# Kernel tuning notes

Hardware: AMD Instinct MI355X
Metric: run time of the kernel (lower is better)

The kernel has to match this reference:

```python
import jax, jax.numpy as jnp
import numpy as np

N, E, G = 50000, 800000, 16
NODE, HID, OUT, HEADS = 128, 64, 128, 3
NEG_SLOPE = 0.2

def setup_inputs() -> dict:
    key = jax.random.key(0)
    ks = jax.random.split(key, 12)
    h = jax.random.normal(ks[0], (N, NODE), jnp.float32)
    z = jax.random.normal(ks[1], (G, OUT), jnp.float32)
    src = jax.random.randint(ks[2], (E,), 0, N, jnp.int32)
    dst = jax.random.randint(ks[3], (E,), 0, N, jnp.int32)
    graph_id = jnp.sort(jax.random.randint(ks[4], (N,), 0, G, jnp.int32))
    s = 0.1
    fc_w = jax.random.normal(ks[5], (HEADS * HID, NODE), jnp.float32) * s
    attn_l = jax.random.normal(ks[6], (HEADS, HID), jnp.float32) * s
    attn_r = jax.random.normal(ks[7], (HEADS, HID), jnp.float32) * s
    bias = jnp.zeros((HEADS * HID,), jnp.float32)
    lin1_w = jax.random.normal(ks[8], (HID, OUT), jnp.float32) * s
    lin1_b = jnp.zeros((HID,), jnp.float32)
    lin2_w = jax.random.normal(ks[9], (1, 2 * HID), jnp.float32) * s
    lin2_b = jnp.zeros((1,), jnp.float32)
    return dict(h=h, z=z, src=src, dst=dst, graph_id=graph_id, fc_w=fc_w,
                attn_l=attn_l, attn_r=attn_r, bias=bias,
                lin1_w=lin1_w, lin1_b=lin1_b, lin2_w=lin2_w, lin2_b=lin2_b)

def reference(h, z, src, dst, graph_id, fc_w, attn_l, attn_r, bias,
              lin1_w, lin1_b, lin2_w, lin2_b):
    n = h.shape[0]
    # GATConv: projection -> [N, H, D]
    feat = (h @ fc_w.T).reshape(n, HEADS, HID)
    el = jnp.sum(feat * attn_l, axis=-1)  # [N, H]
    er = jnp.sum(feat * attn_r, axis=-1)  # [N, H]
    e = jax.nn.leaky_relu(el[src] + er[dst], NEG_SLOPE)  # [E, H]
    # edge softmax per destination node
    m = jax.ops.segment_max(e, dst, num_segments=n)
    e = jnp.exp(e - m[dst])
    s = jax.ops.segment_sum(e, dst, num_segments=n)
    alpha = e / s[dst]
    # scatter-weighted aggregation
    msg = alpha[:, :, None] * feat[src]  # [E, H, D]
    rst = jax.ops.segment_sum(msg, dst, num_segments=n)  # [N, H, D]
    rst = rst + bias.reshape(HEADS, HID)
    h_d = jnp.mean(rst, axis=1)  # [N, D] (mean over heads)
    # dgl.mean_nodes: per-graph mean pooling
    counts = jax.ops.segment_sum(jnp.ones((n,), h_d.dtype), graph_id, num_segments=G)
    pooled = jax.ops.segment_sum(h_d, graph_id, num_segments=G) / jnp.maximum(counts, 1.0)[:, None]
    z1 = z @ lin1_w.T + lin1_b  # [G, HID]
    cat = jnp.concatenate([pooled, z1], axis=1)  # [G, 2*HID]
    score = jax.nn.sigmoid(cat @ lin2_w.T + lin2_b)  # [G, 1]
    return score
```

## Files before the change

kernel.cpp:

```cpp
#include <hip/hip_runtime.h>
#include <math.h>

#define N_NODES 50000
#define N_EDGES 800000
#define N_GRAPHS 16
#define NODE_F 128
#define HID 64
#define OUT_F 128
#define HEADS 3
#define NEG 0.2f
#define FEAT (HEADS*HID)

typedef float f32x4 __attribute__((ext_vector_type(4)));
typedef float f32x2 __attribute__((ext_vector_type(2)));
typedef short bf16x8 __attribute__((ext_vector_type(8)));

#if defined(__has_builtin)
#if __has_builtin(__builtin_amdgcn_cvt_pk_f32_fp8) && __has_builtin(__builtin_amdgcn_cvt_pk_fp8_f32)
#define USE_FP8 1
#endif
#endif
#ifndef USE_FP8
#define USE_FP8 0
#endif

#if USE_FP8
#define FB 1
#else
#define FB 2
#endif
#define GRP (8 * FB)
#define ROW (32 * GRP)

#define NBKT ((N_NODES + 63) / 64)
#define H1B 400
#define EPB (N_EDGES / H1B)

__device__ __forceinline__ ushort f2bf(float x) {
  union { float f; unsigned u; } v; v.f = x;
  unsigned r = v.u + 0x7fff + ((v.u >> 16) & 1);
  return (ushort)(r >> 16);
}
__device__ __forceinline__ float bf2f(ushort x) {
  union { unsigned u; float f; } v; v.u = ((unsigned)x) << 16;
  return v.f;
}

__device__ __forceinline__ void feat_store(unsigned char* base, int n, int hh, int dd, float v) {
  size_t off = (size_t)n * ROW + (dd >> 1) * GRP + ((hh * 2 + (dd & 1)) * FB);
#if USE_FP8
  base[off] = (unsigned char)(__builtin_amdgcn_cvt_pk_fp8_f32(v, 0.f, 0, false) & 0xff);
#else
  *(ushort*)(base + off) = f2bf(v);
#endif
}

#define ZERO_INTS (N_GRAPHS * HID + N_GRAPHS)
#define ZERO_U4 (ZERO_INTS / 4)
#define ZB ((ZERO_U4 + 255) / 256)
__global__ void kprep(const float* __restrict__ fc_w, ushort* __restrict__ fcb,
                      uint4* __restrict__ zbase) {
  if (blockIdx.x >= 24) {
    int i = (blockIdx.x - 24) * 256 + threadIdx.x;
    if (i < ZERO_U4) zbase[i] = make_uint4(0, 0, 0, 0);
    return;
  }
  int i = blockIdx.x * 256 + threadIdx.x;
  int col = i >> 5;
  int kb = (i & 31) * 4;
  float4 v = *(const float4*)(fc_w + (size_t)col * NODE_F + kb);
  int t = col >> 4, m = col & 15;
  int kk = kb >> 5, kq = (kb >> 3) & 3, j = kb & 7;
  size_t idx0 = ((((size_t)t * 4 + kk) * 4 + kq) * 16 + m) * 8 + j;
  ushort4 o; o.x = f2bf(v.x); o.y = f2bf(v.y); o.z = f2bf(v.z); o.w = f2bf(v.w);
  *(ushort4*)(fcb + idx0) = o;
}

#define GB0 ((N_NODES + 63) / 64)
__global__ __launch_bounds__(256) void k01_fused(
    const float* __restrict__ h, const ushort* __restrict__ fcb,
    const float* __restrict__ attn_l, const float* __restrict__ attn_r,
    const int* __restrict__ dst,
    unsigned char* __restrict__ feat, float* __restrict__ el, float* __restrict__ er,
    int* __restrict__ cnt_g)
{
  __shared__ ushort A[64][136];
  const int tid = threadIdx.x;

  if (blockIdx.x < H1B) {
    int* cnt = (int*)&A[0][0];
    const int blk = blockIdx.x;
    for (int i = tid; i < NBKT; i += 256) cnt[i] = 0;
    __syncthreads();
    const int e0 = blk * EPB;
    for (int i = tid; i < EPB; i += 256)
      atomicAdd(&cnt[dst[e0 + i] >> 6], 1);
    __syncthreads();
    for (int i = tid; i < NBKT; i += 256) cnt_g[(size_t)blk * NBKT + i] = cnt[i];
    return;
  }

  const int n0 = (blockIdx.x - H1B) * 64;
  for (int i = tid; i < 64 * 32; i += 256) {
    int r = i >> 5, c4 = i & 31;
    if (n0 + r < N_NODES) {
      float4 v = *(const float4*)(h + (size_t)(n0 + r) * NODE_F + c4 * 4);
      unsigned lo = f2bf(v.x) | ((unsigned)f2bf(v.y) << 16);
      unsigned hi = f2bf(v.z) | ((unsigned)f2bf(v.w) << 16);
      *(uint2*)&A[r][c4 * 4] = make_uint2(lo, hi);
    }
  }
  __syncthreads();

  const int lane = tid & 63, wv = tid >> 6;
  const int m = lane & 15, kq = lane >> 4;

  f32x4 acc[12];
#pragma unroll
  for (int t = 0; t < 12; t++) acc[t] = (f32x4){0.f, 0.f, 0.f, 0.f};

#pragma unroll
  for (int kk = 0; kk < 4; kk++) {
    bf16x8 af = *(const bf16x8*)&A[wv * 16 + m][kk * 32 + kq * 8];
#pragma unroll
    for (int t = 0; t < 12; t++) {
      const bf16x8 bf = *(const bf16x8*)(fcb + ((((size_t)t * 4 + kk) * 4 + kq) * 16 + m) * 8);
      acc[t] = __builtin_amdgcn_mfma_f32_16x16x32_bf16(af, bf, acc[t], 0, 0, 0);
    }
  }

  const int rbase = n0 + wv * 16 + kq * 4;
#pragma unroll
  for (int t = 0; t < 12; t++) {
    const int hh = t >> 2;
    const int dd = (t & 3) * 16 + m;
#pragma unroll
    for (int reg = 0; reg < 4; reg++) {
      int n = rbase + reg;
      if (n < N_NODES) feat_store(feat, n, hh, dd, acc[t][reg]);
    }
  }

#pragma unroll
  for (int hh = 0; hh < HEADS; hh++) {
    float elv[4] = {0.f, 0.f, 0.f, 0.f};
    float erv[4] = {0.f, 0.f, 0.f, 0.f};
#pragma unroll
    for (int tt = 0; tt < 4; tt++) {
      int t = hh * 4 + tt;
      float al = attn_l[hh * HID + tt * 16 + m];
      float ar = attn_r[hh * HID + tt * 16 + m];
#pragma unroll
      for (int reg = 0; reg < 4; reg++) {
        elv[reg] = fmaf(acc[t][reg], al, elv[reg]);
        erv[reg] = fmaf(acc[t][reg], ar, erv[reg]);
      }
    }
#pragma unroll
    for (int reg = 0; reg < 4; reg++) {
#pragma unroll
      for (int off = 1; off < 16; off <<= 1) {
        elv[reg] += __shfl_xor(elv[reg], off, 64);
        erv[reg] += __shfl_xor(erv[reg], off, 64);
      }
      int n = rbase + reg;
      if (m == 0 && n < N_NODES) {
        el[(size_t)n * 4 + hh] = elv[reg];
        er[(size_t)n * 4 + hh] = erv[reg];
      }
    }
  }
}

#define H2A_K 7
__global__ __launch_bounds__(64) void kh2a_scan(
    const int* __restrict__ cnt_g, int* __restrict__ base_bm, int* __restrict__ btot)
{
  const int b = blockIdx.x;
  const int lane = threadIdx.x;
  int v[H2A_K];
  int lt = 0;
#pragma unroll
  for (int j = 0; j < H2A_K; j++) {
    int g = lane * H2A_K + j;
    v[j] = (g < H1B) ? cnt_g[(size_t)g * NBKT + b] : 0;
    lt += v[j];
  }
  int s = lt;
#pragma unroll
  for (int off = 1; off < 64; off <<= 1) {
    int t = __shfl_up(s, off, 64);
    if (lane >= off) s += t;
  }
  int excl = s - lt;
#pragma unroll
  for (int j = 0; j < H2A_K; j++) {
    int g = lane * H2A_K + j;
    if (g < H1B) base_bm[(size_t)b * H1B + g] = excl;
    excl += v[j];
  }
  if (lane == 63) btot[b] = s;
}

__global__ __launch_bounds__(256) void kh3_scatter(
    const int* __restrict__ src, const int* __restrict__ dst,
    const int* __restrict__ btot, const int* __restrict__ base_bm,
    int2* __restrict__ pairs)
{
  __shared__ int cur[NBKT];
  __shared__ int wsum[4];
  const int tid = threadIdx.x, blk = blockIdx.x;
  const int lane = tid & 63, wv = tid >> 6;
  int v[4]; int lt = 0;
#pragma unroll
  for (int j = 0; j < 4; j++) {
    int g = tid * 4 + j;
    v[j] = (g < NBKT) ? btot[g] : 0;
    lt += v[j];
  }
  int s = lt;
#pragma unroll
  for (int off = 1; off < 64; off <<= 1) {
    int t = __shfl_up(s, off, 64);
    if (lane >= off) s += t;
  }
  if (lane == 63) wsum[wv] = s;
  __syncthreads();
  int woff = 0;
#pragma unroll
  for (int w = 0; w < 4; w++) woff += (w < wv) ? wsum[w] : 0;
  int excl = s - lt + woff;
#pragma unroll
  for (int j = 0; j < 4; j++) {
    int g = tid * 4 + j;
    if (g < NBKT) cur[g] = excl + base_bm[(size_t)g * H1B + blk];
    excl += v[j];
  }
  __syncthreads();
  const int e0 = blk * EPB;
  for (int i = tid; i < EPB; i += 256) {
    int e = e0 + i;
    int d = dst[e], sv = src[e];
    int slot = atomicAdd(&cur[d >> 6], 1);
    pairs[slot] = make_int2(sv, d);
  }
}

__global__ __launch_bounds__(256) void kh4_nodesort(
    const int2* __restrict__ pairs, const int* __restrict__ btot,
    int* __restrict__ src_s, int* __restrict__ offs)
{
  __shared__ int nodecnt[64];
  __shared__ int cur[64];
  __shared__ int red_[4];
  __shared__ int lo_s, hi_s;
  const int b = blockIdx.x, tid = threadIdx.x;
  const int lane = tid & 63, wv = tid >> 6;
  int partial = 0;
  for (int i = tid; i < b; i += 256) partial += btot[i];
#pragma unroll
  for (int off = 32; off; off >>= 1) partial += __shfl_xor(partial, off, 64);
  if (lane == 0) red_[wv] = partial;
  if (tid < 64) nodecnt[tid] = 0;
  __syncthreads();
  if (tid == 0) {
    int l = red_[0] + red_[1] + red_[2] + red_[3];
    lo_s = l; hi_s = l + btot[b];
  }
  __syncthreads();
  const int lo = lo_s, hi = hi_s;
  for (int i = lo + tid; i < hi; i += 256)
    atomicAdd(&nodecnt[pairs[i].y & 63], 1);
  __syncthreads();
  if (tid < 64) {
    int v = nodecnt[tid];
    int s = v;
#pragma unroll
    for (int off = 1; off < 64; off <<= 1) {
      int t = __shfl_up(s, off, 64);
      if (tid >= off) s += t;
    }
    int excl = s - v;
    cur[tid] = lo + excl;
    int n = b * 64 + tid;
    if (n < N_NODES) offs[n] = lo + excl;
    if (b == NBKT - 1 && tid == 0) offs[N_NODES] = N_EDGES;
  }
  __syncthreads();
  for (int i = lo + tid; i < hi; i += 256) {
    int2 pr = pairs[i];
    int slot = atomicAdd(&cur[pr.y & 63], 1);
    src_s[slot] = pr.x;
  }
}

__global__ __launch_bounds__(256) void k4_agg(
    const int* __restrict__ offs, const int* __restrict__ src_s,
    const float* __restrict__ el4, const float* __restrict__ er4,
    const unsigned char* __restrict__ feat, const float* __restrict__ bias,
    float* __restrict__ h_d)
{
  __shared__ float4 rec[4][64];
  const int wv = threadIdx.x >> 6, lane = threadIdx.x & 63;
  const int n = blockIdx.x * 4 + wv;
  const int lo = offs[n], hi = offs[n + 1];
  const int half = lane >> 5;
  const int d = lane & 31;
  const char* fb = (const char*)feat;
  const float4 ern = ((const float4*)er4)[n];

  float a0x = 0.f, a0y = 0.f, a1x = 0.f, a1y = 0.f, a2x = 0.f, a2y = 0.f;
  float s0 = 0.f, s1 = 0.f, s2 = 0.f;

  for (int base = lo; base < hi; base += 64) {
    const int cnt = min(64, hi - base);
    if (lane < cnt) {
      int sidx = src_s[base + lane];
      float4 elv = ((const float4*)el4)[sidx];
      float e0 = elv.x + ern.x; e0 = e0 > 0.f ? e0 : NEG * e0;
      float e1 = elv.y + ern.y; e1 = e1 > 0.f ? e1 : NEG * e1;
      float e2 = elv.z + ern.z; e2 = e2 > 0.f ? e2 : NEG * e2;
      float4 c;
      c.x = __expf(e0); c.y = __expf(e1); c.z = __expf(e2);
      c.w = __int_as_float(sidx * ROW);
      rec[wv][lane] = c;
      s0 += c.x; s1 += c.y; s2 += c.z;
    }
#define K4_BODY(J) do { \
      float4 c = rec[wv][J]; \
      const char* rp = fb + __float_as_int(c.w) + GRP * d; \
      f32x2 f0, f1, f2; \
      if (USE_FP8) { \
        uint2 q = *(const uint2*)rp; \
        f0 = __builtin_amdgcn_cvt_pk_f32_fp8(q.x & 0xffff, false); \
        f1 = __builtin_amdgcn_cvt_pk_f32_fp8(q.x >> 16, false); \
        f2 = __builtin_amdgcn_cvt_pk_f32_fp8(q.y & 0xffff, false); \
      } else { \
        uint4 q = *(const uint4*)rp; \
        f0.x = bf2f((ushort)(q.x & 0xffff)); f0.y = bf2f((ushort)(q.x >> 16)); \
        f1.x = bf2f((ushort)(q.y & 0xffff)); f1.y = bf2f((ushort)(q.y >> 16)); \
        f2.x = bf2f((ushort)(q.z & 0xffff)); f2.y = bf2f((ushort)(q.z >> 16)); \
      } \
      a0x = fmaf(c.x, f0.x, a0x); a0y = fmaf(c.x, f0.y, a0y); \
      a1x = fmaf(c.y, f1.x, a1x); a1y = fmaf(c.y, f1.y, a1y); \
      a2x = fmaf(c.z, f2.x, a2x); a2y = fmaf(c.z, f2.y, a2y); \
    } while (0)
    int j = half;
    for (; j + 2 < cnt; j += 4) { K4_BODY(j); K4_BODY(j + 2); }
    if (j < cnt) K4_BODY(j);
#undef K4_BODY
  }
  a0x += __shfl_xor(a0x, 32, 64); a0y += __shfl_xor(a0y, 32, 64);
  a1x += __shfl_xor(a1x, 32, 64); a1y += __shfl_xor(a1y, 32, 64);
  a2x += __shfl_xor(a2x, 32, 64); a2y += __shfl_xor(a2y, 32, 64);
#pragma unroll
  for (int off = 32; off; off >>= 1) {
    s0 += __shfl_xor(s0, off, 64);
    s1 += __shfl_xor(s1, off, 64);
    s2 += __shfl_xor(s2, off, 64);
  }
  const float i0 = s0 > 0.f ? 1.f / s0 : 0.f;
  const float i1 = s1 > 0.f ? 1.f / s1 : 0.f;
  const float i2 = s2 > 0.f ? 1.f / s2 : 0.f;
  if (half == 0) {
    float2 b0 = *(const float2*)(bias + 2 * d);
    float2 b1 = *(const float2*)(bias + HID + 2 * d);
    float2 b2 = *(const float2*)(bias + 2 * HID + 2 * d);
    float2 o;
    o.x = (fmaf(a0x, i0, b0.x) + fmaf(a1x, i1, b1.x) + fmaf(a2x, i2, b2.x)) * (1.f / 3.f);
    o.y = (fmaf(a0y, i0, b0.y) + fmaf(a1y, i1, b1.y) + fmaf(a2y, i2, b2.y)) * (1.f / 3.f);
    *(float2*)(h_d + (size_t)n * HID + 2 * d) = o;
  }
}

#define K5_NPB 128
#define K5_NB ((N_NODES + K5_NPB - 1) / K5_NPB)
#define NSEG (K5_NB * 2)
__global__ __launch_bounds__(256) void k5a_partial(
    const int* __restrict__ graph_id, const float* __restrict__ h_d,
    float* __restrict__ pooled_res, int* __restrict__ gcnt_res,
    float* __restrict__ part, int* __restrict__ pg, int* __restrict__ pc)
{
  const int wv = threadIdx.x >> 6, lane = threadIdx.x & 63;
  const int b = blockIdx.x;
  const int n0 = b * K5_NPB;
  const int n1 = min(n0 + K5_NPB, N_NODES);
  const int g_lo = graph_id[n0], g_hi = graph_id[n1 - 1];

  if (g_hi > g_lo + 1) {
    float acc = 0.f; int cur_g = -1; int cnt = 0;
    for (int i = n0 + wv; i < n1; i += 4) {
      int g = graph_id[i];
      if (g != cur_g) {
        if (cur_g >= 0) {
          atomicAdd(&pooled_res[cur_g * HID + lane], acc);
          if (lane == 0) atomicAdd(&gcnt_res[cur_g], cnt);
        }
        acc = 0.f; cnt = 0; cur_g = g;
      }
      acc += h_d[(size_t)i * HID + lane];
      cnt++;
    }
    if (cur_g >= 0) {
      atomicAdd(&pooled_res[cur_g * HID + lane], acc);
      if (lane == 0) atomicAdd(&gcnt_res[cur_g], cnt);
    }
    if (threadIdx.x < 2) pg[b * 2 + threadIdx.x] = -1;
    return;
  }

  float acc_lo = 0.f, acc_hi = 0.f;
  int c_lo = 0, c_hi = 0;
  for (int i = n0 + wv; i < n1; i += 4) {
    int g = graph_id[i];
    float v = h_d[(size_t)i * HID + lane];
    bool hi = (g != g_lo);
    acc_hi += hi ? v : 0.f;
    acc_lo += hi ? 0.f : v;
    c_hi += hi ? 1 : 0;
    c_lo += hi ? 0 : 1;
  }
  __shared__ float ls[2][4][64];
  __shared__ int lc[2][4];
  ls[0][wv][lane] = acc_lo;
  ls[1][wv][lane] = acc_hi;
  if (lane == 0) { lc[0][wv] = c_lo; lc[1][wv] = c_hi; }
  __syncthreads();
  if (wv < 2) {
    float s = ls[wv][0][lane] + ls[wv][1][lane] + ls[wv][2][lane] + ls[wv][3][lane];
    part[((size_t)b * 2 + wv) * HID + lane] = s;
    if (lane == 0) {
      int cnt = lc[wv][0] + lc[wv][1] + lc[wv][2] + lc[wv][3];
      int gg = (wv == 0) ? g_lo : g_hi;
      if (wv == 1 && (g_hi == g_lo || cnt == 0)) gg = -1;
      pg[b * 2 + wv] = gg;
      pc[b * 2 + wv] = cnt;
    }
  }
}

__global__ __launch_bounds__(256) void k6_final(
    const float* __restrict__ part, const int* __restrict__ pg, const int* __restrict__ pc,
    const float* __restrict__ pooled_res, const int* __restrict__ gcnt_res,
    const float* __restrict__ z,
    const float* __restrict__ lin1_w, const float* __restrict__ lin1_b,
    const float* __restrict__ lin2_w, const float* __restrict__ lin2_b,
    float* __restrict__ out)
{
  const int g = blockIdx.x;
  const int tid = threadIdx.x, wv = tid >> 6, lane = tid & 63;
  __shared__ int spg[NSEG], spc[NSEG];
  __shared__ float red[4][HID];
  __shared__ int rc[4];
  __shared__ float cat[2 * HID];

  for (int i = tid; i < NSEG; i += 256) { spg[i] = pg[i]; spc[i] = pc[i]; }
  __syncthreads();

  float acc = 0.f; int cnt = 0;
  for (int s = wv; s < NSEG; s += 4) {
    if (spg[s] == g) {
      acc += part[(size_t)s * HID + lane];
      cnt += spc[s];
    }
  }
  red[wv][lane] = acc;
  if (lane == 0) rc[wv] = cnt;
  __syncthreads();

  if (wv == 0) {
    float s = red[0][lane] + red[1][lane] + red[2][lane] + red[3][lane]
            + pooled_res[g * HID + lane];
    int c = rc[0] + rc[1] + rc[2] + rc[3] + gcnt_res[g];
    cat[lane] = s / (float)(c > 0 ? c : 1);
  }
  if (wv == 1) {
    float s = lin1_b[lane];
    const float* zr = z + g * OUT_F;
    const float* wr = lin1_w + lane * OUT_F;
    for (int k = 0; k < OUT_F; k += 4) {
      float4 zv = *(const float4*)(zr + k);
      float4 wv4 = *(const float4*)(wr + k);
      s = fmaf(zv.x, wv4.x, fmaf(zv.y, wv4.y, fmaf(zv.z, wv4.z, fmaf(zv.w, wv4.w, s))));
    }
    cat[HID + lane] = s;
  }
  __syncthreads();
  if (wv == 0) {
    float s = cat[lane] * lin2_w[lane] + cat[HID + lane] * lin2_w[HID + lane];
#pragma unroll
    for (int off = 32; off; off >>= 1) s += __shfl_xor(s, off, 64);
    if (lane == 0) out[g] = 1.f / (1.f + __expf(-(s + lin2_b[0])));
  }
}

extern "C" void kernel_launch(void* const* d_in, const int* in_sizes, int n_in,
                              void* d_out, int out_size, void* d_ws, size_t ws_size,
                              hipStream_t stream) {
  (void)in_sizes; (void)n_in; (void)out_size; (void)ws_size;
  const float* h      = (const float*)d_in[0];
  const float* z      = (const float*)d_in[1];
  const int*   src    = (const int*)d_in[2];
  const int*   dst    = (const int*)d_in[3];
  const int*   gid    = (const int*)d_in[4];
  const float* fc_w   = (const float*)d_in[5];
  const float* attn_l = (const float*)d_in[6];
  const float* attn_r = (const float*)d_in[7];
  const float* bias   = (const float*)d_in[8];
  const float* lin1_w = (const float*)d_in[9];
  const float* lin1_b = (const float*)d_in[10];
  const float* lin2_w = (const float*)d_in[11];
  const float* lin2_b = (const float*)d_in[12];
  float* out = (float*)d_out;

  int2* pairs       = (int2*)d_ws;
  unsigned char* feat = (unsigned char*)(pairs + N_EDGES);
  float* h_d        = (float*)(feat + (size_t)N_NODES * ROW);
  float* el         = h_d + (size_t)N_NODES * HID;
  float* er         = el + (size_t)N_NODES * 4;
  float* part       = er + (size_t)N_NODES * 4;
  int* pg           = (int*)(part + (size_t)NSEG * HID);
  int* pc           = pg + NSEG;
  ushort* fcb       = (ushort*)(pc + NSEG);
  float* pooled_res = (float*)(fcb + 192 * NODE_F);
  int* gcnt_res     = (int*)(pooled_res + N_GRAPHS * HID);
  int* offs         = gcnt_res + N_GRAPHS;
  int* src_s        = offs + (N_NODES + 1);
  int* cnt_g        = src_s + N_EDGES;
  int* base_bm      = cnt_g + (size_t)H1B * NBKT;
  int* btot         = base_bm + (size_t)NBKT * H1B;

  kprep<<<24 + ZB, 256, 0, stream>>>(fc_w, fcb, (uint4*)pooled_res);
  k01_fused<<<H1B + GB0, 256, 0, stream>>>(h, fcb, attn_l, attn_r, dst,
                                           feat, el, er, cnt_g);
  kh2a_scan<<<NBKT, 64, 0, stream>>>(cnt_g, base_bm, btot);
  kh3_scatter<<<H1B, 256, 0, stream>>>(src, dst, btot, base_bm, pairs);
  kh4_nodesort<<<NBKT, 256, 0, stream>>>(pairs, btot, src_s, offs);
  k4_agg<<<N_NODES / 4, 256, 0, stream>>>(offs, src_s, el, er, feat, bias, h_d);
  k5a_partial<<<K5_NB, 256, 0, stream>>>(gid, h_d, pooled_res, gcnt_res, part, pg, pc);
  k6_final<<<N_GRAPHS, 256, 0, stream>>>(part, pg, pc, pooled_res, gcnt_res,
                                         z, lin1_w, lin1_b, lin2_w, lin2_b, out);
}
```

Measured before the change: 206.1 us.

## Fuse node sort, aggregation and pooling into one bucket-per-block kernel

```diff
diff --git a/kernel.cpp b/kernel.cpp
--- a/kernel.cpp
+++ b/kernel.cpp
@@ -35,6 +35,8 @@
 #define NBKT ((N_NODES + 63) / 64)
 #define H1B 400
 #define EPB (N_EDGES / H1B)
+#define NSEG (NBKT * 2)
+#define MAXE 2048
 
 __device__ __forceinline__ ushort f2bf(float x) {
   union { float f; unsigned u; } v; v.f = x;
@@ -246,31 +248,52 @@
   }
 }
 
-__global__ __launch_bounds__(256) void kh4_nodesort(
+#define K4W 8
+__global__ __launch_bounds__(512) void k4_big(
     const int2* __restrict__ pairs, const int* __restrict__ btot,
-    int* __restrict__ src_s, int* __restrict__ offs)
+    const int* __restrict__ gid,
+    const float* __restrict__ el4, const float* __restrict__ er4,
+    const unsigned char* __restrict__ feat, const float* __restrict__ bias,
+    float* __restrict__ pooled_res, int* __restrict__ gcnt_res,
+    float* __restrict__ part, int* __restrict__ pg, int* __restrict__ pc,
+    int* __restrict__ src_ovf)
 {
-  __shared__ int nodecnt[64];
-  __shared__ int cur[64];
-  __shared__ int red_[4];
-  __shared__ int lo_s, hi_s;
+  __shared__ int ssrc[MAXE];
+  __shared__ int nodecnt[64], noff[64], cur[64];
+  __shared__ int red_[K4W];
+  __shared__ int lo_s;
+  __shared__ float4 rec[K4W][64];
+  __shared__ float pool[K4W][2][HID];
+  __shared__ int pooln[K4W][2];
   const int b = blockIdx.x, tid = threadIdx.x;
   const int lane = tid & 63, wv = tid >> 6;
+
   int partial = 0;
-  for (int i = tid; i < b; i += 256) partial += btot[i];
+  for (int i = tid; i < b; i += 512) partial += btot[i];
 #pragma unroll
   for (int off = 32; off; off >>= 1) partial += __shfl_xor(partial, off, 64);
   if (lane == 0) red_[wv] = partial;
   if (tid < 64) nodecnt[tid] = 0;
+  if (tid < 64) { pool[tid >> 6][0][lane] = 0.f; }
   __syncthreads();
   if (tid == 0) {
-    int l = red_[0] + red_[1] + red_[2] + red_[3];
-    lo_s = l; hi_s = l + btot[b];
-  }
-  __syncthreads();
-  const int lo = lo_s, hi = hi_s;
-  for (int i = lo + tid; i < hi; i += 256)
-    atomicAdd(&nodecnt[pairs[i].y & 63], 1);
+    int l = 0;
+#pragma unroll
+    for (int w = 0; w < K4W; w++) l += red_[w];
+    lo_s = l;
+  }
+  if (tid < 512) {
+    int w = tid >> 6;
+    pool[w][0][lane] = 0.f;
+    pool[w][1][lane] = 0.f;
+    if (lane == 0) { pooln[w][0] = 0; pooln[w][1] = 0; }
+  }
+  __syncthreads();
+  const int lo = lo_s;
+  const int cnt = btot[b];
+
+  for (int i = tid; i < cnt; i += 512)
+    atomicAdd(&nodecnt[pairs[lo + i].y & 63], 1);
   __syncthreads();
   if (tid < 64) {
     int v = nodecnt[tid];
@@ -280,52 +303,54 @@
       int t = __shfl_up(s, off, 64);
       if (tid >= off) s += t;
     }
-    int excl = s - v;
-    cur[tid] = lo + excl;
-    int n = b * 64 + tid;
-    if (n < N_NODES) offs[n] = lo + excl;
-    if (b == NBKT - 1 && tid == 0) offs[N_NODES] = N_EDGES;
-  }
-  __syncthreads();
-  for (int i = lo + tid; i < hi; i += 256) {
-    int2 pr = pairs[i];
+    noff[tid] = s - v;
+    cur[tid] = s - v;
+  }
+  __syncthreads();
+  int* slist = (cnt <= MAXE) ? (int*)ssrc : (src_ovf + lo);
+  for (int i = tid; i < cnt; i += 512) {
+    int2 pr = pairs[lo + i];
     int slot = atomicAdd(&cur[pr.y & 63], 1);
-    src_s[slot] = pr.x;
-  }
-}
-
-__global__ __launch_bounds__(256) void k4_agg(
-    const int* __restrict__ offs, const int* __restrict__ src_s,
-    const float* __restrict__ el4, const float* __restrict__ er4,
-    const unsigned char* __restrict__ feat, const float* __restrict__ bias,
-    float* __restrict__ h_d)
-{
-  __shared__ float4 rec[4][64];
-  const int wv = threadIdx.x >> 6, lane = threadIdx.x & 63;
-  const int n = blockIdx.x * 4 + wv;
-  const int lo = offs[n], hi = offs[n + 1];
+    slist[slot] = pr.x;
+  }
+  __syncthreads();
+
+  const int g_lo = gid[b * 64];
+  const int nlast = min(b * 64 + 63, N_NODES - 1);
+  const int g_hi = gid[nlast];
+  const bool rare = (g_hi > g_lo + 1);
+
   const int half = lane >> 5;
   const int d = lane & 31;
   const char* fb = (const char*)feat;
-  const float4 ern = ((const float4*)er4)[n];
-
-  float a0x = 0.f, a0y = 0.f, a1x = 0.f, a1y = 0.f, a2x = 0.f, a2y = 0.f;
-  float s0 = 0.f, s1 = 0.f, s2 = 0.f;
-
-  for (int base = lo; base < hi; base += 64) {
-    const int cnt = min(64, hi - base);
-    if (lane < cnt) {
-      int sidx = src_s[base + lane];
-      float4 elv = ((const float4*)el4)[sidx];
-      float e0 = elv.x + ern.x; e0 = e0 > 0.f ? e0 : NEG * e0;
-      float e1 = elv.y + ern.y; e1 = e1 > 0.f ? e1 : NEG * e1;
-      float e2 = elv.z + ern.z; e2 = e2 > 0.f ? e2 : NEG * e2;
-      float4 c;
-      c.x = __expf(e0); c.y = __expf(e1); c.z = __expf(e2);
-      c.w = __int_as_float(sidx * ROW);
-      rec[wv][lane] = c;
-      s0 += c.x; s1 += c.y; s2 += c.z;
-    }
+  const float2 b0 = *(const float2*)(bias + 2 * d);
+  const float2 b1 = *(const float2*)(bias + HID + 2 * d);
+  const float2 b2 = *(const float2*)(bias + 2 * HID + 2 * d);
+
+  for (int nl = wv; nl < 64; nl += K4W) {
+    const int n = b * 64 + nl;
+    if (n >= N_NODES) break;
+    const int elo = noff[nl];
+    const int ecnt = nodecnt[nl];
+    const float4 ern = ((const float4*)er4)[n];
+
+    float a0x = 0.f, a0y = 0.f, a1x = 0.f, a1y = 0.f, a2x = 0.f, a2y = 0.f;
+    float s0 = 0.f, s1 = 0.f, s2 = 0.f;
+
+    for (int base2 = elo; base2 < elo + ecnt; base2 += 64) {
+      const int c2 = min(64, elo + ecnt - base2);
+      if (lane < c2) {
+        int sidx = slist[base2 + lane];
+        float4 elv = ((const float4*)el4)[sidx];
+        float e0 = elv.x + ern.x; e0 = e0 > 0.f ? e0 : NEG * e0;
+        float e1 = elv.y + ern.y; e1 = e1 > 0.f ? e1 : NEG * e1;
+        float e2 = elv.z + ern.z; e2 = e2 > 0.f ? e2 : NEG * e2;
+        float4 c;
+        c.x = __expf(e0); c.y = __expf(e1); c.z = __expf(e2);
+        c.w = __int_as_float(sidx * ROW);
+        rec[wv][lane] = c;
+        s0 += c.x; s1 += c.y; s2 += c.z;
+      }
 #define K4_BODY(J) do { \
       float4 c = rec[wv][J]; \
       const char* rp = fb + __float_as_int(c.w) + GRP * d; \
@@ -345,96 +370,56 @@
       a1x = fmaf(c.y, f1.x, a1x); a1y = fmaf(c.y, f1.y, a1y); \
       a2x = fmaf(c.z, f2.x, a2x); a2y = fmaf(c.z, f2.y, a2y); \
     } while (0)
-    int j = half;
-    for (; j + 2 < cnt; j += 4) { K4_BODY(j); K4_BODY(j + 2); }
-    if (j < cnt) K4_BODY(j);
+      int j = half;
+      for (; j + 2 < c2; j += 4) { K4_BODY(j); K4_BODY(j + 2); }
+      if (j < c2) K4_BODY(j);
 #undef K4_BODY
-  }
-  a0x += __shfl_xor(a0x, 32, 64); a0y += __shfl_xor(a0y, 32, 64);
-  a1x += __shfl_xor(a1x, 32, 64); a1y += __shfl_xor(a1y, 32, 64);
-  a2x += __shfl_xor(a2x, 32, 64); a2y += __shfl_xor(a2y, 32, 64);
-#pragma unroll
-  for (int off = 32; off; off >>= 1) {
-    s0 += __shfl_xor(s0, off, 64);
-    s1 += __shfl_xor(s1, off, 64);
-    s2 += __shfl_xor(s2, off, 64);
-  }
-  const float i0 = s0 > 0.f ? 1.f / s0 : 0.f;
-  const float i1 = s1 > 0.f ? 1.f / s1 : 0.f;
-  const float i2 = s2 > 0.f ? 1.f / s2 : 0.f;
-  if (half == 0) {
-    float2 b0 = *(const float2*)(bias + 2 * d);
-    float2 b1 = *(const float2*)(bias + HID + 2 * d);
-    float2 b2 = *(const float2*)(bias + 2 * HID + 2 * d);
-    float2 o;
-    o.x = (fmaf(a0x, i0, b0.x) + fmaf(a1x, i1, b1.x) + fmaf(a2x, i2, b2.x)) * (1.f / 3.f);
-    o.y = (fmaf(a0y, i0, b0.y) + fmaf(a1y, i1, b1.y) + fmaf(a2y, i2, b2.y)) * (1.f / 3.f);
-    *(float2*)(h_d + (size_t)n * HID + 2 * d) = o;
-  }
-}
-
-#define K5_NPB 128
-#define K5_NB ((N_NODES + K5_NPB - 1) / K5_NPB)
-#define NSEG (K5_NB * 2)
-__global__ __launch_bounds__(256) void k5a_partial(
-    const int* __restrict__ graph_id, const float* __restrict__ h_d,
-    float* __restrict__ pooled_res, int* __restrict__ gcnt_res,
-    float* __restrict__ part, int* __restrict__ pg, int* __restrict__ pc)
-{
-  const int wv = threadIdx.x >> 6, lane = threadIdx.x & 63;
-  const int b = blockIdx.x;
-  const int n0 = b * K5_NPB;
-  const int n1 = min(n0 + K5_NPB, N_NODES);
-  const int g_lo = graph_id[n0], g_hi = graph_id[n1 - 1];
-
-  if (g_hi > g_lo + 1) {
-    float acc = 0.f; int cur_g = -1; int cnt = 0;
-    for (int i = n0 + wv; i < n1; i += 4) {
-      int g = graph_id[i];
-      if (g != cur_g) {
-        if (cur_g >= 0) {
-          atomicAdd(&pooled_res[cur_g * HID + lane], acc);
-          if (lane == 0) atomicAdd(&gcnt_res[cur_g], cnt);
-        }
-        acc = 0.f; cnt = 0; cur_g = g;
+    }
+    a0x += __shfl_xor(a0x, 32, 64); a0y += __shfl_xor(a0y, 32, 64);
+    a1x += __shfl_xor(a1x, 32, 64); a1y += __shfl_xor(a1y, 32, 64);
+    a2x += __shfl_xor(a2x, 32, 64); a2y += __shfl_xor(a2y, 32, 64);
+#pragma unroll
+    for (int off = 32; off; off >>= 1) {
+      s0 += __shfl_xor(s0, off, 64);
+      s1 += __shfl_xor(s1, off, 64);
+      s2 += __shfl_xor(s2, off, 64);
+    }
+    const float i0 = s0 > 0.f ? 1.f / s0 : 0.f;
+    const float i1 = s1 > 0.f ? 1.f / s1 : 0.f;
+    const float i2 = s2 > 0.f ? 1.f / s2 : 0.f;
+    if (half == 0) {
+      float ox = (fmaf(a0x, i0, b0.x) + fmaf(a1x, i1, b1.x) + fmaf(a2x, i2, b2.x)) * (1.f / 3.f);
+      float oy = (fmaf(a0y, i0, b0.y) + fmaf(a1y, i1, b1.y) + fmaf(a2y, i2, b2.y)) * (1.f / 3.f);
+      if (!rare) {
+        int hi = (gid[n] != g_lo) ? 1 : 0;
+        pool[wv][hi][2 * d]     += ox;
+        pool[wv][hi][2 * d + 1] += oy;
+        if (d == 0) pooln[wv][hi]++;
+      } else {
+        int g = gid[n];
+        atomicAdd(&pooled_res[g * HID + 2 * d], ox);
+        atomicAdd(&pooled_res[g * HID + 2 * d + 1], oy);
+        if (d == 0) atomicAdd(&gcnt_res[g], 1);
       }
-      acc += h_d[(size_t)i * HID + lane];
-      cnt++;
-    }
-    if (cur_g >= 0) {
-      atomicAdd(&pooled_res[cur_g * HID + lane], acc);
-      if (lane == 0) atomicAdd(&gcnt_res[cur_g], cnt);
-    }
-    if (threadIdx.x < 2) pg[b * 2 + threadIdx.x] = -1;
-    return;
-  }
-
-  float acc_lo = 0.f, acc_hi = 0.f;
-  int c_lo = 0, c_hi = 0;
-  for (int i = n0 + wv; i < n1; i += 4) {
-    int g = graph_id[i];
-    float v = h_d[(size_t)i * HID + lane];
-    bool hi = (g != g_lo);
-    acc_hi += hi ? v : 0.f;
-    acc_lo += hi ? 0.f : v;
-    c_hi += hi ? 1 : 0;
-    c_lo += hi ? 0 : 1;
-  }
-  __shared__ float ls[2][4][64];
-  __shared__ int lc[2][4];
-  ls[0][wv][lane] = acc_lo;
-  ls[1][wv][lane] = acc_hi;
-  if (lane == 0) { lc[0][wv] = c_lo; lc[1][wv] = c_hi; }
-  __syncthreads();
-  if (wv < 2) {
-    float s = ls[wv][0][lane] + ls[wv][1][lane] + ls[wv][2][lane] + ls[wv][3][lane];
-    part[((size_t)b * 2 + wv) * HID + lane] = s;
-    if (lane == 0) {
-      int cnt = lc[wv][0] + lc[wv][1] + lc[wv][2] + lc[wv][3];
-      int gg = (wv == 0) ? g_lo : g_hi;
-      if (wv == 1 && (g_hi == g_lo || cnt == 0)) gg = -1;
-      pg[b * 2 + wv] = gg;
-      pc[b * 2 + wv] = cnt;
+    }
+  }
+  __syncthreads();
+  if (tid < 128) {
+    int sub = tid >> 6;
+    int l = tid & 63;
+    float s = 0.f;
+#pragma unroll
+    for (int w = 0; w < K4W; w++) s += pool[w][sub][l];
+    part[((size_t)b * 2 + sub) * HID + l] = s;
+    if (l == 0) {
+      int c = 0;
+#pragma unroll
+      for (int w = 0; w < K4W; w++) c += pooln[w][sub];
+      int gg = (sub == 0) ? g_lo : g_hi;
+      if (rare) gg = -1;
+      if (sub == 1 && (g_hi == g_lo || c == 0)) gg = -1;
+      pg[b * 2 + sub] = gg;
+      pc[b * 2 + sub] = c;
     }
   }
 }
@@ -515,8 +500,7 @@
 
   int2* pairs       = (int2*)d_ws;
   unsigned char* feat = (unsigned char*)(pairs + N_EDGES);
-  float* h_d        = (float*)(feat + (size_t)N_NODES * ROW);
-  float* el         = h_d + (size_t)N_NODES * HID;
+  float* el         = (float*)(feat + (size_t)N_NODES * ROW);
   float* er         = el + (size_t)N_NODES * 4;
   float* part       = er + (size_t)N_NODES * 4;
   int* pg           = (int*)(part + (size_t)NSEG * HID);
@@ -524,20 +508,18 @@
   ushort* fcb       = (ushort*)(pc + NSEG);
   float* pooled_res = (float*)(fcb + 192 * NODE_F);
   int* gcnt_res     = (int*)(pooled_res + N_GRAPHS * HID);
-  int* offs         = gcnt_res + N_GRAPHS;
-  int* src_s        = offs + (N_NODES + 1);
-  int* cnt_g        = src_s + N_EDGES;
+  int* cnt_g        = gcnt_res + N_GRAPHS;
   int* base_bm      = cnt_g + (size_t)H1B * NBKT;
   int* btot         = base_bm + (size_t)NBKT * H1B;
+  int* src_ovf      = btot + NBKT;
 
   kprep<<<24 + ZB, 256, 0, stream>>>(fc_w, fcb, (uint4*)pooled_res);
   k01_fused<<<H1B + GB0, 256, 0, stream>>>(h, fcb, attn_l, attn_r, dst,
                                            feat, el, er, cnt_g);
   kh2a_scan<<<NBKT, 64, 0, stream>>>(cnt_g, base_bm, btot);
   kh3_scatter<<<H1B, 256, 0, stream>>>(src, dst, btot, base_bm, pairs);
-  kh4_nodesort<<<NBKT, 256, 0, stream>>>(pairs, btot, src_s, offs);
-  k4_agg<<<N_NODES / 4, 256, 0, stream>>>(offs, src_s, el, er, feat, bias, h_d);
-  k5a_partial<<<K5_NB, 256, 0, stream>>>(gid, h_d, pooled_res, gcnt_res, part, pg, pc);
+  k4_big<<<NBKT, 512, 0, stream>>>(pairs, btot, gid, el, er, feat, bias,
+                                   pooled_res, gcnt_res, part, pg, pc, src_ovf);
   k6_final<<<N_GRAPHS, 256, 0, stream>>>(part, pg, pc, pooled_res, gcnt_res,
                                          z, lin1_w, lin1_b, lin2_w, lin2_b, out);
 }
```

Measured after the change: 230.6 us. 11.9% more time.
